# Kernel optimization log

Measured on AMD Instinct MI355X. Metric: run time of the kernel, lower is better.

## Reference

```python
import jax, jax.numpy as jnp
import numpy as np

N_NODES = 50000


def gcn_conv(x, W, b, edge_index, n_nodes):
    """torch_geometric GCNConv: linear -> symmetric-normalized scatter-add with self-loops."""
    h = x @ W  # [N, out]
    src = jnp.concatenate([edge_index[0], jnp.arange(n_nodes)])  # add self-loops
    dst = jnp.concatenate([edge_index[1], jnp.arange(n_nodes)])
    deg = jax.ops.segment_sum(jnp.ones_like(dst, dtype=h.dtype), dst, num_segments=n_nodes)
    dinv = jnp.where(deg > 0, jax.lax.rsqrt(deg), 0.0)  # deg^-1/2, inf -> 0
    norm = dinv[src] * dinv[dst]                         # [E+N]
    msg = h[src] * norm[:, None]                         # gather + scale
    out = jax.ops.segment_sum(msg, dst, num_segments=n_nodes)  # scatter-add
    return out + b


def setup_inputs() -> dict:
    key = jax.random.key(0)
    k1, k2, k3, k4, k5, k6 = jax.random.split(key, 6)
    nhid, nfeat = 128, 256
    E = 800000
    x = jax.random.normal(k1, (N_NODES, nhid), dtype=jnp.float32)
    edge_index = jax.random.randint(k2, (2, E), 0, N_NODES, dtype=jnp.int64)
    s1 = 1.0 / np.sqrt(nhid)
    W1 = jax.random.uniform(k3, (nhid, nhid), jnp.float32, -s1, s1)
    b1 = jnp.zeros((nhid,), jnp.float32)
    W2 = jax.random.uniform(k4, (nhid, nfeat), jnp.float32, -s1, s1)
    b2 = jnp.zeros((nfeat,), jnp.float32)
    return {"x": x, "edge_index": edge_index, "W1": W1, "b1": b1, "W2": W2, "b2": b2}


def reference(x, edge_index, W1, b1, W2, b2):
    # eval mode: dropout is identity
    h = jax.nn.relu(gcn_conv(x, W1, b1, edge_index, N_NODES))
    out = jax.nn.relu(gcn_conv(h, W2, b2, edge_index, N_NODES))
    return out
```

## Files before the change

### kernel.cpp

```cpp
#include <hip/hip_runtime.h>


typedef __attribute__((ext_vector_type(8))) _Float16 half8;
typedef __attribute__((ext_vector_type(4))) _Float16 half4v;
typedef __attribute__((ext_vector_type(4))) float floatx4;

#define BSHIFT 7
#define BNODES 128
#define BCAP   4096

__global__ __launch_bounds__(256) void scatter_conv_kernel(const int* __restrict__ src,
                                                           const int* __restrict__ dst,
                                                           int* __restrict__ bucket_fill,
                                                           unsigned* __restrict__ bucketed,
                                                           const float* __restrict__ W1,
                                                           const float* __restrict__ W2,
                                                           _Float16* __restrict__ wt1,
                                                           _Float16* __restrict__ wt2,
                                                           int E, int chunk, int NB) {
    int t = threadIdx.x;
    if (blockIdx.x >= 256) {
        int idx = (blockIdx.x - 256) * 256 + t;
        if (idx < 128 * 128) {
            int nn = idx >> 7, k = idx & 127;
            wt1[idx] = (_Float16)W1[k * 128 + nn];
        } else if (idx < (128 + 256) * 128) {
            int j = idx - 128 * 128;
            int nn = j >> 7, k = j & 127;
            wt2[j] = (_Float16)W2[k * 256 + nn];
        }
        return;
    }
    extern __shared__ int sh[];
    int* hist = sh;
    int* base_loc = sh + NB;
    int* cur2 = sh + 2 * NB;
    for (int i = t; i < NB; i += 256) { hist[i] = 0; cur2[i] = 0; }
    __syncthreads();
    int cbeg = blockIdx.x * chunk;
    int cend = min(E, cbeg + chunk);
    for (int e = cbeg + t; e < cend; e += 256)
        atomicAdd(&hist[dst[e] >> BSHIFT], 1);
    __syncthreads();
    for (int i = t; i < NB; i += 256) {
        int c = hist[i];
        base_loc[i] = c ? atomicAdd(&bucket_fill[i], c) : 0;
    }
    __syncthreads();
    for (int e = cbeg + t; e < cend; e += 256) {
        int d = dst[e];
        int bkt = d >> BSHIFT;
        int r = atomicAdd(&cur2[bkt], 1);
        bucketed[(size_t)bkt * BCAP + base_loc[bkt] + r] =
            (unsigned)src[e] | ((unsigned)(d & (BNODES - 1)) << 16);
    }
}

__global__ __launch_bounds__(256) void build_kernel(const unsigned* __restrict__ bucketed,
                                                    const int* __restrict__ bucket_fill,
                                                    const float* __restrict__ x,
                                                    int* __restrict__ rowstart,
                                                    int* __restrict__ rowend,
                                                    float* __restrict__ dinv,
                                                    int* __restrict__ csr,
                                                    _Float16* __restrict__ xs,
                                                    int N, int NB) {
    __shared__ int deg_loc[BNODES];
    __shared__ int tmp[BNODES];
    __shared__ int cur_loc[BNODES];
    __shared__ float dinv_loc[BNODES];
    int t = threadIdx.x;
    int b = blockIdx.x;
    int n0 = b << BSHIFT;
    int nodes_in = min(BNODES, N - n0);
    size_t wbase = (size_t)b * BCAP;
    int cnt = bucket_fill[b];

    if (t < BNODES) deg_loc[t] = 0;
    __syncthreads();
    for (int e = t; e < cnt; e += 256)
        atomicAdd(&deg_loc[bucketed[wbase + e] >> 16], 1);
    __syncthreads();
    if (t < BNODES) tmp[t] = deg_loc[t];
    __syncthreads();
    for (int off = 1; off < BNODES; off <<= 1) {
        int v = 0;
        if (t < BNODES && t >= off) v = tmp[t - off];
        __syncthreads();
        if (t < BNODES) tmp[t] += v;
        __syncthreads();
    }
    if (t < BNODES) {
        int abs0 = (int)wbase + tmp[t] - deg_loc[t];
        cur_loc[t] = abs0;
        float dv = rsqrtf((float)(deg_loc[t] + 1));
        dinv_loc[t] = dv;
        if (t < nodes_in) {
            rowstart[n0 + t] = abs0;
            rowend[n0 + t] = abs0 + deg_loc[t];
            dinv[n0 + t] = dv;
        }
    }
    __syncthreads();
    for (int e = t; e < cnt; e += 256) {
        unsigned u2 = bucketed[wbase + e];
        int pos = atomicAdd(&cur_loc[u2 >> 16], 1);
        csr[pos] = (int)(u2 & 0xFFFFu);
    }
    int total4 = nodes_in * 32;
    const float4* x4 = (const float4*)(x + (size_t)n0 * 128);
    for (int i = t; i < total4; i += 256) {
        int row = i >> 5;
        float dv = dinv_loc[row];
        float4 v = x4[i];
        half4v h;
        h[0] = (_Float16)(v.x * dv); h[1] = (_Float16)(v.y * dv);
        h[2] = (_Float16)(v.z * dv); h[3] = (_Float16)(v.w * dv);
        *(half4v*)(xs + (size_t)n0 * 128 + (size_t)i * 4) = h;
    }
}

__global__ __launch_bounds__(256) void agg128_kernel(const _Float16* __restrict__ g,
                                                     const int* __restrict__ rowstart,
                                                     const int* __restrict__ rowend,
                                                     const float* __restrict__ dinv,
                                                     const int* __restrict__ csr,
                                                     _Float16* __restrict__ out, int n) {
    int wave = (blockIdx.x * blockDim.x + threadIdx.x) >> 6;
    int lane = threadIdx.x & 63;
    int q = lane >> 4, l16 = lane & 15;
    int node = wave * 4 + q;
    if (node >= n) return;
    int beg = rowstart[node], end = rowend[node];

    float a[8];
    {
        half8 v = *(const half8*)(g + (size_t)node * 128 + l16 * 8);
#pragma unroll
        for (int j = 0; j < 8; j++) a[j] = (float)v[j];
    }
    int e = beg;
    for (; e + 7 < end; e += 8) {
        int u0 = csr[e],     u1 = csr[e + 1], u2 = csr[e + 2], u3 = csr[e + 3];
        int u4 = csr[e + 4], u5 = csr[e + 5], u6 = csr[e + 6], u7 = csr[e + 7];
        half8 v0 = *(const half8*)(g + (size_t)u0 * 128 + l16 * 8);
        half8 v1 = *(const half8*)(g + (size_t)u1 * 128 + l16 * 8);
        half8 v2 = *(const half8*)(g + (size_t)u2 * 128 + l16 * 8);
        half8 v3 = *(const half8*)(g + (size_t)u3 * 128 + l16 * 8);
        half8 v4 = *(const half8*)(g + (size_t)u4 * 128 + l16 * 8);
        half8 v5 = *(const half8*)(g + (size_t)u5 * 128 + l16 * 8);
        half8 v6 = *(const half8*)(g + (size_t)u6 * 128 + l16 * 8);
        half8 v7 = *(const half8*)(g + (size_t)u7 * 128 + l16 * 8);
#pragma unroll
        for (int j = 0; j < 8; j++)
            a[j] += (((float)v0[j] + (float)v1[j]) + ((float)v2[j] + (float)v3[j])) +
                    (((float)v4[j] + (float)v5[j]) + ((float)v6[j] + (float)v7[j]));
    }
    for (; e + 3 < end; e += 4) {
        int u0 = csr[e], u1 = csr[e + 1], u2 = csr[e + 2], u3 = csr[e + 3];
        half8 v0 = *(const half8*)(g + (size_t)u0 * 128 + l16 * 8);
        half8 v1 = *(const half8*)(g + (size_t)u1 * 128 + l16 * 8);
        half8 v2 = *(const half8*)(g + (size_t)u2 * 128 + l16 * 8);
        half8 v3 = *(const half8*)(g + (size_t)u3 * 128 + l16 * 8);
#pragma unroll
        for (int j = 0; j < 8; j++)
            a[j] += ((float)v0[j] + (float)v1[j]) + ((float)v2[j] + (float)v3[j]);
    }
    for (; e < end; e++) {
        int u = csr[e];
        half8 v = *(const half8*)(g + (size_t)u * 128 + l16 * 8);
#pragma unroll
        for (int j = 0; j < 8; j++) a[j] += (float)v[j];
    }
    float dv = dinv[node];
    half8 o;
#pragma unroll
    for (int j = 0; j < 8; j++) o[j] = (_Float16)(a[j] * dv);
    *(half8*)(out + (size_t)node * 128 + l16 * 8) = o;
}

template <bool HALF_OUT>
__global__ __launch_bounds__(256) void gemm_kernel(const _Float16* __restrict__ A,
                                                   const _Float16* __restrict__ Bt,
                                                   const float* __restrict__ bias,
                                                   const float* __restrict__ dinv,
                                                   void* __restrict__ outp,
                                                   int n, int nout) {
    __shared__ _Float16 As[128][136];
    __shared__ _Float16 Bs[128][136];
    int t = threadIdx.x;
    int row0 = blockIdx.x * 128;
    int col0 = blockIdx.y * 128;

#pragma unroll
    for (int i = 0; i < 8; i++) {
        int c = i * 256 + t;
        int r = c >> 4, seg = c & 15;
        int gr = row0 + r;
        if (gr >= n) gr = n - 1;
        uint4 v = *(const uint4*)(A + (size_t)gr * 128 + seg * 8);
        *(uint4*)(&As[r][seg * 8]) = v;
    }
#pragma unroll
    for (int i = 0; i < 8; i++) {
        int c = i * 256 + t;
        int r = c >> 4, seg = c & 15;
        uint4 v = *(const uint4*)(Bt + (size_t)(col0 + r) * 128 + seg * 8);
        *(uint4*)(&Bs[r][seg * 8]) = v;
    }
    __syncthreads();

    int wid = t >> 6, lane = t & 63;
    int wm = wid >> 1, wn = wid & 1;
    int quad = lane >> 4, l16 = lane & 15;

    floatx4 acc[4][4];
#pragma unroll
    for (int mt = 0; mt < 4; mt++)
#pragma unroll
        for (int nt = 0; nt < 4; nt++) acc[mt][nt] = (floatx4){0.f, 0.f, 0.f, 0.f};

#pragma unroll
    for (int ks = 0; ks < 4; ks++) {
        int k0 = ks * 32 + quad * 8;
        half8 a[4], b[4];
#pragma unroll
        for (int mt = 0; mt < 4; mt++)
            a[mt] = *(const half8*)(&As[wm * 64 + mt * 16 + l16][k0]);
#pragma unroll
        for (int nt = 0; nt < 4; nt++)
            b[nt] = *(const half8*)(&Bs[wn * 64 + nt * 16 + l16][k0]);
#pragma unroll
        for (int mt = 0; mt < 4; mt++)
#pragma unroll
            for (int nt = 0; nt < 4; nt++)
                acc[mt][nt] = __builtin_amdgcn_mfma_f32_16x16x32_f16(a[mt], b[nt], acc[mt][nt], 0, 0, 0);
    }

#pragma unroll
    for (int mt = 0; mt < 4; mt++) {
        int rbase = row0 + wm * 64 + mt * 16 + quad * 4;
#pragma unroll
        for (int reg = 0; reg < 4; reg++) {
            int r = rbase + reg;
            if (r < n) {
                float dv = HALF_OUT ? dinv[r] : 1.f;
#pragma unroll
                for (int nt = 0; nt < 4; nt++) {
                    int cc = col0 + wn * 64 + nt * 16 + l16;
                    float val = fmaxf(acc[mt][nt][reg] + bias[cc], 0.f);
                    if (HALF_OUT)
                        ((_Float16*)outp)[(size_t)r * nout + cc] = (_Float16)(val * dv);
                    else
                        ((float*)outp)[(size_t)r * nout + cc] = val;
                }
            }
        }
    }
}

extern "C" void kernel_launch(void* const* d_in, const int* in_sizes, int n_in,
                              void* d_out, int out_size, void* d_ws, size_t ws_size,
                              hipStream_t stream) {
    const float* x  = (const float*)d_in[0];
    const int*   ei = (const int*)d_in[1];
    const float* W1 = (const float*)d_in[2];
    const float* b1 = (const float*)d_in[3];
    const float* W2 = (const float*)d_in[4];
    const float* b2 = (const float*)d_in[5];
    float* out = (float*)d_out;

    int N = in_sizes[0] / 128;
    int E = in_sizes[1] / 2;
    const int* src = ei;
    const int* dst = ei + E;
    int NB = (N + BNODES - 1) >> BSHIFT;

    char* w = (char*)d_ws;
    size_t off = 0;
    auto alloc = [&](size_t bytes) -> char* {
        char* p = w + off;
        off = (off + bytes + 255) & ~(size_t)255;
        return p;
    };
    int*      bucket_fill = (int*)alloc((size_t)NB * 4);
    unsigned* bucketed    = (unsigned*)alloc((size_t)NB * BCAP * 4);
    int*      rowstart    = (int*)alloc((size_t)N * 4);
    int*      rowend      = (int*)alloc((size_t)N * 4);
    float*    dinv        = (float*)alloc((size_t)N * 4);
    int*      csr         = (int*)alloc((size_t)NB * BCAP * 4);
    _Float16* wt1         = (_Float16*)alloc((size_t)128 * 128 * 2);
    _Float16* wt2         = (_Float16*)alloc((size_t)256 * 128 * 2);
    _Float16* xs          = (_Float16*)alloc((size_t)N * 128 * 2);
    _Float16* q1          = (_Float16*)alloc((size_t)N * 128 * 2);
    _Float16* p2          = (_Float16*)alloc((size_t)N * 128 * 2);
    _Float16* q2          = (_Float16*)alloc((size_t)N * 128 * 2);

    int chunk = (E + 255) / 256;
    size_t lds3 = (size_t)NB * 12;

    hipMemsetAsync(bucket_fill, 0, (size_t)NB * 4, stream);
    hipLaunchKernelGGL(scatter_conv_kernel, dim3(256 + 192), dim3(256), lds3, stream,
                       src, dst, bucket_fill, bucketed, W1, W2, wt1, wt2, E, chunk, NB);
    hipLaunchKernelGGL(build_kernel, dim3(NB), dim3(256), 0, stream,
                       bucketed, bucket_fill, x, rowstart, rowend, dinv, csr, xs, N, NB);

    int gbm = (N + 127) / 128;
    int nwave = (N + 3) / 4;
    int nb_agg = (nwave * 64 + 255) / 256;
    hipLaunchKernelGGL(agg128_kernel, dim3(nb_agg), dim3(256), 0, stream, xs, rowstart, rowend, dinv, csr, q1, N);
    hipLaunchKernelGGL((gemm_kernel<true>), dim3(gbm, 1), dim3(256), 0, stream, q1, wt1, b1, dinv, (void*)p2, N, 128);
    hipLaunchKernelGGL(agg128_kernel, dim3(nb_agg), dim3(256), 0, stream, p2, rowstart, rowend, dinv, csr, q2, N);
    hipLaunchKernelGGL((gemm_kernel<false>), dim3(gbm, 2), dim3(256), 0, stream, q2, wt2, b2, dinv, (void*)out, N, 256);
}
```

Before: 212.8 us.

## Split feature aggregation into four 32-column passes for cache locality

```diff
diff --git a/kernel.cpp b/kernel.cpp
--- a/kernel.cpp
+++ b/kernel.cpp
@@ -3,6 +3,7 @@
 
 typedef __attribute__((ext_vector_type(8))) _Float16 half8;
 typedef __attribute__((ext_vector_type(4))) _Float16 half4v;
+typedef __attribute__((ext_vector_type(2))) _Float16 half2v;
 typedef __attribute__((ext_vector_type(4))) float floatx4;
 
 #define BSHIFT 7
@@ -120,63 +121,61 @@
     }
 }
 
-__global__ __launch_bounds__(256) void agg128_kernel(const _Float16* __restrict__ g,
-                                                     const int* __restrict__ rowstart,
-                                                     const int* __restrict__ rowend,
-                                                     const float* __restrict__ dinv,
-                                                     const int* __restrict__ csr,
-                                                     _Float16* __restrict__ out, int n) {
+__global__ __launch_bounds__(256) void agg32_kernel(const _Float16* __restrict__ g,
+                                                    const int* __restrict__ rowstart,
+                                                    const int* __restrict__ rowend,
+                                                    const float* __restrict__ dinv,
+                                                    const int* __restrict__ csr,
+                                                    _Float16* __restrict__ out,
+                                                    int n, int s32) {
     int wave = (blockIdx.x * blockDim.x + threadIdx.x) >> 6;
     int lane = threadIdx.x & 63;
     int q = lane >> 4, l16 = lane & 15;
     int node = wave * 4 + q;
     if (node >= n) return;
     int beg = rowstart[node], end = rowend[node];
-
-    float a[8];
+    const _Float16* gs = g + s32 + l16 * 2;
+
+    float a0, a1;
     {
-        half8 v = *(const half8*)(g + (size_t)node * 128 + l16 * 8);
-#pragma unroll
-        for (int j = 0; j < 8; j++) a[j] = (float)v[j];
+        half2v v = *(const half2v*)(gs + (size_t)node * 128);
+        a0 = (float)v[0]; a1 = (float)v[1];
     }
     int e = beg;
     for (; e + 7 < end; e += 8) {
         int u0 = csr[e],     u1 = csr[e + 1], u2 = csr[e + 2], u3 = csr[e + 3];
         int u4 = csr[e + 4], u5 = csr[e + 5], u6 = csr[e + 6], u7 = csr[e + 7];
-        half8 v0 = *(const half8*)(g + (size_t)u0 * 128 + l16 * 8);
-        half8 v1 = *(const half8*)(g + (size_t)u1 * 128 + l16 * 8);
-        half8 v2 = *(const half8*)(g + (size_t)u2 * 128 + l16 * 8);
-        half8 v3 = *(const half8*)(g + (size_t)u3 * 128 + l16 * 8);
-        half8 v4 = *(const half8*)(g + (size_t)u4 * 128 + l16 * 8);
-        half8 v5 = *(const half8*)(g + (size_t)u5 * 128 + l16 * 8);
-        half8 v6 = *(const half8*)(g + (size_t)u6 * 128 + l16 * 8);
-        half8 v7 = *(const half8*)(g + (size_t)u7 * 128 + l16 * 8);
-#pragma unroll
-        for (int j = 0; j < 8; j++)
-            a[j] += (((float)v0[j] + (float)v1[j]) + ((float)v2[j] + (float)v3[j])) +
-                    (((float)v4[j] + (float)v5[j]) + ((float)v6[j] + (float)v7[j]));
+        half2v v0 = *(const half2v*)(gs + (size_t)u0 * 128);
+        half2v v1 = *(const half2v*)(gs + (size_t)u1 * 128);
+        half2v v2 = *(const half2v*)(gs + (size_t)u2 * 128);
+        half2v v3 = *(const half2v*)(gs + (size_t)u3 * 128);
+        half2v v4 = *(const half2v*)(gs + (size_t)u4 * 128);
+        half2v v5 = *(const half2v*)(gs + (size_t)u5 * 128);
+        half2v v6 = *(const half2v*)(gs + (size_t)u6 * 128);
+        half2v v7 = *(const half2v*)(gs + (size_t)u7 * 128);
+        a0 += (((float)v0[0] + (float)v1[0]) + ((float)v2[0] + (float)v3[0])) +
+              (((float)v4[0] + (float)v5[0]) + ((float)v6[0] + (float)v7[0]));
+        a1 += (((float)v0[1] + (float)v1[1]) + ((float)v2[1] + (float)v3[1])) +
+              (((float)v4[1] + (float)v5[1]) + ((float)v6[1] + (float)v7[1]));
     }
     for (; e + 3 < end; e += 4) {
         int u0 = csr[e], u1 = csr[e + 1], u2 = csr[e + 2], u3 = csr[e + 3];
-        half8 v0 = *(const half8*)(g + (size_t)u0 * 128 + l16 * 8);
-        half8 v1 = *(const half8*)(g + (size_t)u1 * 128 + l16 * 8);
-        half8 v2 = *(const half8*)(g + (size_t)u2 * 128 + l16 * 8);
-        half8 v3 = *(const half8*)(g + (size_t)u3 * 128 + l16 * 8);
-#pragma unroll
-        for (int j = 0; j < 8; j++)
-            a[j] += ((float)v0[j] + (float)v1[j]) + ((float)v2[j] + (float)v3[j]);
+        half2v v0 = *(const half2v*)(gs + (size_t)u0 * 128);
+        half2v v1 = *(const half2v*)(gs + (size_t)u1 * 128);
+        half2v v2 = *(const half2v*)(gs + (size_t)u2 * 128);
+        half2v v3 = *(const half2v*)(gs + (size_t)u3 * 128);
+        a0 += ((float)v0[0] + (float)v1[0]) + ((float)v2[0] + (float)v3[0]);
+        a1 += ((float)v0[1] + (float)v1[1]) + ((float)v2[1] + (float)v3[1]);
     }
     for (; e < end; e++) {
         int u = csr[e];
-        half8 v = *(const half8*)(g + (size_t)u * 128 + l16 * 8);
-#pragma unroll
-        for (int j = 0; j < 8; j++) a[j] += (float)v[j];
+        half2v v = *(const half2v*)(gs + (size_t)u * 128);
+        a0 += (float)v[0]; a1 += (float)v[1];
     }
     float dv = dinv[node];
-    half8 o;
-#pragma unroll
-    for (int j = 0; j < 8; j++) o[j] = (_Float16)(a[j] * dv);
-    *(half8*)(out + (size_t)node * 128 + l16 * 8) = o;
+    half2v o;
+    o[0] = (_Float16)(a0 * dv); o[1] = (_Float16)(a1 * dv);
+    *(half2v*)(out + (size_t)node * 128 + s32 + l16 * 2) = o;
 }
 
 template <bool HALF_OUT>
@@ -308,8 +307,12 @@
     int gbm = (N + 127) / 128;
     int nwave = (N + 3) / 4;
     int nb_agg = (nwave * 64 + 255) / 256;
-    hipLaunchKernelGGL(agg128_kernel, dim3(nb_agg), dim3(256), 0, stream, xs, rowstart, rowend, dinv, csr, q1, N);
+    for (int s = 0; s < 4; s++)
+        hipLaunchKernelGGL(agg32_kernel, dim3(nb_agg), dim3(256), 0, stream,
+                           xs, rowstart, rowend, dinv, csr, q1, N, s * 32);
     hipLaunchKernelGGL((gemm_kernel<true>), dim3(gbm, 1), dim3(256), 0, stream, q1, wt1, b1, dinv, (void*)p2, N, 128);
-    hipLaunchKernelGGL(agg128_kernel, dim3(nb_agg), dim3(256), 0, stream, p2, rowstart, rowend, dinv, csr, q2, N);
+    for (int s = 0; s < 4; s++)
+        hipLaunchKernelGGL(agg32_kernel, dim3(nb_agg), dim3(256), 0, stream,
+                           p2, rowstart, rowend, dinv, csr, q2, N, s * 32);
     hipLaunchKernelGGL((gemm_kernel<false>), dim3(gbm, 2), dim3(256), 0, stream, q2, wt2, b2, dinv, (void*)out, N, 256);
 }
```

After: 275.7 us. 29.6% more time.
